# Optimization experiments

Hardware: AMD Instinct MI355X
Metric: run time of the kernel (lower is better)

The kernel has to match this reference:

```python
import jax, jax.numpy as jnp
import numpy as np

B, T, E, NH, VOCAB, MULT = 1, 1024, 768, 12, 32000, 32
N = E * MULT // NH  # 2048
LN_EPS = 1e-5


def setup_inputs() -> dict:
    key = jax.random.key(0)
    ks = jax.random.split(key, 6)
    return {
        "idx": jax.random.randint(ks[0], (B, T), 0, VOCAB),
        "embed": jax.random.normal(ks[1], (VOCAB, E), jnp.float32) * 0.02,
        "encoder": jax.random.normal(ks[2], (NH, E, N), jnp.float32) * 0.02,
        "encoder_v": jax.random.normal(ks[3], (NH, E, N), jnp.float32) * 0.02,
        "decoder": jax.random.normal(ks[4], (NH * N, E), jnp.float32) * 0.02,
        "lm_head": jax.random.normal(ks[5], (VOCAB, E), jnp.float32) * 0.02,
        "ln_w": jnp.ones((E,), jnp.float32),
        "ln_b": jnp.zeros((E,), jnp.float32),
        "n_layer": 6,
    }


def reference(idx, embed, encoder, encoder_v, decoder, lm_head, ln_w, ln_b, n_layer):
    nh, e, n = encoder.shape
    t = idx.shape[1]
    dec = decoder.reshape(nh, n, e)  # flatten order (h, n) -> h*N + n

    def ln(x):
        m = jnp.mean(x, axis=-1, keepdims=True)
        v = jnp.mean(jnp.square(x - m), axis=-1, keepdims=True)
        return (x - m) * jax.lax.rsqrt(v + LN_EPS) * ln_w + ln_b

    causal = jnp.tril(jnp.ones((t, t), bool))  # [T, T]
    scale = 1.0 / np.sqrt(n).astype(np.float32)

    x = ln(embed[idx])  # [B, T, E]  (the unsqueezed head dim broadcasts; keep it squeezed)
    for _ in range(n_layer):
        # encoder projection + ReLU: [B,T,E] x [H,E,N] -> [B,H,T,N]
        x_sparse = jax.nn.relu(jnp.einsum("bte,hen->bhtn", x, encoder))
        # hand-rolled causal attention, Q=K=x_sparse, V=x (broadcast over heads)
        scores = jnp.einsum("bhqn,bhkn->bhqk", x_sparse, x_sparse) * scale
        scores = jnp.where(causal, scores, -jnp.inf)
        attn = jax.nn.softmax(scores, axis=-1)
        y = jnp.einsum("bhqk,bke->bhqe", attn, x)  # [B,H,T,E]
        y = ln(y)
        y_sparse = jax.nn.relu(jnp.einsum("bhte,hen->bhtn", y, encoder_v))
        xy = x_sparse * y_sparse  # [B,H,T,N]; dropout p=0 -> identity
        y_mlp = jnp.einsum("bhtn,hne->bte", xy, dec)  # decoder matmul
        x = ln(x + ln(y_mlp))
    logits = jnp.einsum("bte,ve->btv", x, lm_head)
    return logits
```

## Files before the change

kernel.cpp:

```cpp
#include <hip/hip_runtime.h>

typedef unsigned short u16;
typedef short bf16x8 __attribute__((ext_vector_type(8)));
typedef float f32x4 __attribute__((ext_vector_type(4)));
typedef u16 u16x4 __attribute__((ext_vector_type(4)));

#define TT     1024
#define EE     768
#define NHH    12
#define ND     2048
#define VOC    32000
#define HNN    24576
#define NLAYER 6
#define LN_EPS 1e-5f
#define SPLITK 16

__device__ __forceinline__ float b2f(u16 u){
  unsigned int x = ((unsigned int)u) << 16; float f; __builtin_memcpy(&f, &x, 4); return f;
}
__device__ __forceinline__ u16 f2b(float f){
  unsigned int x; __builtin_memcpy(&x, &f, 4);
  x = x + 0x7fffu + ((x >> 16) & 1u);
  return (u16)(x >> 16);
}

__device__ __forceinline__ void gload16(const void* g, void* lds){
  __builtin_amdgcn_global_load_lds(
      (const __attribute__((address_space(1))) unsigned int*)g,
      (__attribute__((address_space(3))) unsigned int*)(unsigned int)(unsigned long long)lds,
      16, 0, 0);
}

__device__ __forceinline__ bf16x8 ldsr(unsigned addr){
  bf16x8 r;
  asm volatile("ds_read_b128 %0, %1" : "=v"(r) : "v"(addr));
  return r;
}

__device__ __forceinline__ void blk_sum2(float& a, float& b){
  #pragma unroll
  for (int o = 32; o > 0; o >>= 1){ a += __shfl_down(a, o); b += __shfl_down(b, o); }
  __shared__ float sa[4], sb[4];
  int lane = threadIdx.x & 63, wid = threadIdx.x >> 6;
  __syncthreads();
  if (lane == 0){ sa[wid] = a; sb[wid] = b; }
  __syncthreads();
  a = (sa[0] + sa[1]) + (sa[2] + sa[3]);
  b = (sb[0] + sb[1]) + (sb[2] + sb[3]);
}
__device__ __forceinline__ float blk_max(float v){
  #pragma unroll
  for (int o = 32; o > 0; o >>= 1) v = fmaxf(v, __shfl_down(v, o));
  __shared__ float sm[4];
  int lane = threadIdx.x & 63, wid = threadIdx.x >> 6;
  __syncthreads();
  if (lane == 0) sm[wid] = v;
  __syncthreads();
  return fmaxf(fmaxf(sm[0], sm[1]), fmaxf(sm[2], sm[3]));
}
__device__ __forceinline__ float blk_sum(float v){
  #pragma unroll
  for (int o = 32; o > 0; o >>= 1) v += __shfl_down(v, o);
  __shared__ float ss[4];
  int lane = threadIdx.x & 63, wid = threadIdx.x >> 6;
  __syncthreads();
  if (lane == 0) ss[wid] = v;
  __syncthreads();
  return (ss[0] + ss[1]) + (ss[2] + ss[3]);
}

__global__ void prep(const float* __restrict__ enc, const float* __restrict__ encv,
                     const float* __restrict__ dec, const float* __restrict__ lmh,
                     u16* __restrict__ encT, u16* __restrict__ encvT,
                     u16* __restrict__ decT, u16* __restrict__ lmhB){
  __shared__ float tile[32][33];
  int b = blockIdx.x;
  int lx = threadIdx.x & 31, ly = threadIdx.x >> 5;
  if (b < 36864){
    const float* in; u16* out;
    if (b < 18432){ in = enc; out = encT; } else { in = encv; out = encvT; b -= 18432; }
    int z = b / 1536, rem = b - z * 1536;
    int c0 = (rem & 63) * 32, r0 = (rem >> 6) * 32;
    in  += (long)z * EE * ND;
    out += (long)z * ND * EE;
    #pragma unroll
    for (int i = 0; i < 32; i += 8)
      tile[ly + i][lx] = in[(long)(r0 + ly + i) * ND + c0 + lx];
    __syncthreads();
    #pragma unroll
    for (int i = 0; i < 32; i += 8)
      out[(long)(c0 + ly + i) * EE + r0 + lx] = f2b(tile[lx][ly + i]);
  } else if (b < 55296){
    b -= 36864;
    int c0 = (b % 24) * 32, r0 = (b / 24) * 32;
    #pragma unroll
    for (int i = 0; i < 32; i += 8)
      tile[ly + i][lx] = dec[(long)(r0 + ly + i) * EE + c0 + lx];
    __syncthreads();
    #pragma unroll
    for (int i = 0; i < 32; i += 8)
      decT[(long)(c0 + ly + i) * HNN + r0 + lx] = f2b(tile[lx][ly + i]);
  } else {
    b -= 55296;
    long i = ((long)b * 256 + threadIdx.x) * 4;
    float4 v = *(const float4*)(lmh + i);
    u16x4 o; o.x = f2b(v.x); o.y = f2b(v.y); o.z = f2b(v.z); o.w = f2b(v.w);
    *(u16x4*)(lmhB + i) = o;
  }
}

__global__ void xpose(const u16* __restrict__ in, u16* __restrict__ out){
  __shared__ u16 t[64][65];
  int e0 = blockIdx.x * 64, t0 = blockIdx.y * 64;
  int lx = threadIdx.x & 63, ly = threadIdx.x >> 6;
  #pragma unroll
  for (int i = 0; i < 64; i += 4)
    t[ly + i][lx] = in[(long)(t0 + ly + i) * EE + e0 + lx];
  __syncthreads();
  #pragma unroll
  for (int i = 0; i < 64; i += 4)
    out[(long)(e0 + ly + i) * TT + t0 + lx] = t[lx][ly + i];
}

__global__ void embed_ln(const int* __restrict__ idx, const float* __restrict__ emb,
                         const float* __restrict__ w, const float* __restrict__ b,
                         float* __restrict__ xf, u16* __restrict__ xb){
  int t = blockIdx.x, tid = threadIdx.x;
  const float* src = emb + (long)idx[t] * EE;
  float v[4] = {0.f, 0.f, 0.f, 0.f};
  if (tid < 192){
    float4 r = *(const float4*)&src[tid * 4];
    v[0] = r.x; v[1] = r.y; v[2] = r.z; v[3] = r.w;
  }
  float s = (v[0] + v[1]) + (v[2] + v[3]);
  float s2 = (v[0]*v[0] + v[1]*v[1]) + (v[2]*v[2] + v[3]*v[3]);
  blk_sum2(s, s2);
  float m  = s * (1.0f / EE);
  float var = s2 * (1.0f / EE) - m * m;
  float rs = rsqrtf(var + LN_EPS);
  if (tid < 192){
    int e0 = tid * 4;
    float4 o; u16x4 ob;
    float* op = &o.x;
    #pragma unroll
    for (int j = 0; j < 4; j++){
      float ov = (v[j] - m) * rs * w[e0 + j] + b[e0 + j];
      op[j] = ov; ob[j] = f2b(ov);
    }
    *(float4*)&xf[(long)t * EE + e0] = o;
    *(u16x4*)&xb[(long)t * EE + e0] = ob;
  }
}

__global__ void ln_rows(const u16* __restrict__ in, u16* __restrict__ out,
                        const float* __restrict__ w, const float* __restrict__ b){
  long row = blockIdx.x; int tid = threadIdx.x;
  const u16* src = in + row * EE;
  float v[4] = {0.f, 0.f, 0.f, 0.f};
  if (tid < 192){
    u16x4 r = *(const u16x4*)&src[tid * 4];
    #pragma unroll
    for (int j = 0; j < 4; j++) v[j] = b2f(r[j]);
  }
  float s = (v[0] + v[1]) + (v[2] + v[3]);
  float s2 = (v[0]*v[0] + v[1]*v[1]) + (v[2]*v[2] + v[3]*v[3]);
  blk_sum2(s, s2);
  float m = s * (1.0f / EE);
  float var = s2 * (1.0f / EE) - m * m;
  float rs = rsqrtf(var + LN_EPS);
  if (tid < 192){
    int e0 = tid * 4;
    u16x4 ob;
    #pragma unroll
    for (int j = 0; j < 4; j++) ob[j] = f2b((v[j] - m) * rs * w[e0 + j] + b[e0 + j]);
    *(u16x4*)&out[row * EE + e0] = ob;
  }
}

__global__ void softmax_rows(const u16* __restrict__ scores, u16* __restrict__ attn){
  int q = blockIdx.x, h = blockIdx.y, tid = threadIdx.x;
  const u16* srow = scores + ((long)h * TT + q) * TT;
  u16* arow = attn + ((long)h * TT + q) * TT;
  const int len = q + 1;
  const int pad = (q + 128) & ~127;
  u16x4 raw = *(const u16x4*)&srow[tid * 4];
  float v[4];
  float mx = -1e30f;
  #pragma unroll
  for (int j = 0; j < 4; j++){
    int i = tid * 4 + j;
    v[j] = (i < len) ? b2f(raw[j]) : -1e30f;
    mx = fmaxf(mx, v[j]);
  }
  mx = blk_max(mx);
  float s = 0.f;
  #pragma unroll
  for (int j = 0; j < 4; j++){
    int i = tid * 4 + j;
    float e = (i < len) ? __expf(v[j] - mx) : 0.f;
    v[j] = e; s += e;
  }
  float inv = 1.0f / blk_sum(s);
  int i0 = tid * 4;
  if (i0 < pad){
    u16x4 o;
    #pragma unroll
    for (int j = 0; j < 4; j++) o[j] = (i0 + j < len) ? f2b(v[j] * inv) : (u16)0;
    *(u16x4*)&arow[i0] = o;
  }
}

template<int P>
__global__ void residual_ln(const u16* __restrict__ part, const float* __restrict__ xin,
                            float* __restrict__ xf, u16* __restrict__ xb,
                            const float* __restrict__ w, const float* __restrict__ b){
  int t = blockIdx.x, tid = threadIdx.x;
  float g[4] = {0.f, 0.f, 0.f, 0.f};
  if (tid < 192){
    int e0 = tid * 4;
    #pragma unroll
    for (int pp = 0; pp < P; pp++){
      u16x4 r = *(const u16x4*)&part[((long)pp * TT + t) * EE + e0];
      #pragma unroll
      for (int j = 0; j < 4; j++) g[j] += b2f(r[j]);
    }
  }
  float s = (g[0] + g[1]) + (g[2] + g[3]);
  float s2 = (g[0]*g[0] + g[1]*g[1]) + (g[2]*g[2] + g[3]*g[3]);
  blk_sum2(s, s2);
  float m = s * (1.0f / EE), var = s2 * (1.0f / EE) - m * m;
  float rs = rsqrtf(var + LN_EPS);
  float hh[4] = {0.f, 0.f, 0.f, 0.f};
  if (tid < 192){
    int e0 = tid * 4;
    float4 xi = *(const float4*)&xin[(long)t * EE + e0];
    const float* xp = &xi.x;
    #pragma unroll
    for (int j = 0; j < 4; j++)
      hh[j] = xp[j] + ((g[j] - m) * rs * w[e0 + j] + b[e0 + j]);
  }
  s = (hh[0] + hh[1]) + (hh[2] + hh[3]);
  s2 = (hh[0]*hh[0] + hh[1]*hh[1]) + (hh[2]*hh[2] + hh[3]*hh[3]);
  blk_sum2(s, s2);
  m = s * (1.0f / EE); var = s2 * (1.0f / EE) - m * m; rs = rsqrtf(var + LN_EPS);
  if (tid < 192){
    int e0 = tid * 4;
    float4 o; u16x4 ob;
    float* op = &o.x;
    #pragma unroll
    for (int j = 0; j < 4; j++){
      float ov = (hh[j] - m) * rs * w[e0 + j] + b[e0 + j];
      op[j] = ov; ob[j] = f2b(ov);
    }
    *(float4*)&xf[(long)t * EE + e0] = o;
    *(u16x4*)&xb[(long)t * EE + e0] = ob;
  }
}

template<int EPI>
__global__ __launch_bounds__(512, 2)
void g8(const u16* __restrict__ Ab, long sA,
        const u16* __restrict__ Bb, long sB,
        void* __restrict__ Cb, long sC,
        int grid_m, int grid_mn,
        int K, int lda, int ldb, int ldc, float scale,
        const u16* __restrict__ Mul, long sMul, int ldmul){
  __shared__ __align__(16) u16 S[65536];

  const int nwg = gridDim.x, orig = blockIdx.x;
  const int q = nwg >> 3, r = nwg & 7, xcd = orig & 7;
  const int wgid = (xcd < r ? xcd*(q+1) : r*(q+1) + (xcd - r)*q) + (orig >> 3);
  const int z   = wgid / grid_mn;
  const int rem = wgid - z*grid_mn;
  const int nb  = rem / grid_m;
  const int mb  = rem - nb*grid_m;
  const int m0 = mb*256, n0 = nb*256;
  const int tid = threadIdx.x, lane = tid & 63, wid = tid >> 6;

  if (EPI == 2 && n0 > m0 + 255) return;

  const u16* A = Ab + (long)z*sA;
  const u16* B = Bb + (long)z*sB;

  const int rS = wid*16 + (lane >> 2);
  const int cS = (((lane & 3) ^ ((rS >> 1) & 3)) << 3);
  const u16* gA = A + (long)(m0 + rS)*lda + cS;
  const u16* gB = B + (long)(n0 + rS)*ldb + cS;

  char* Sb = (char*)&S[0];
  const unsigned db0 = 0, db1 = 65536u;
  auto issue = [&](const u16* src, unsigned dstOff){
    gload16(src, Sb + dstOff + (unsigned)wid*1024u);
  };

  const int wr = wid >> 2, wc = wid & 3;
  const int fr = lane & 15, fk = lane >> 4;
  const unsigned base = (unsigned)(unsigned long long)Sb;
  unsigned aOff[8], bOff[4];
  #pragma unroll
  for (int mi = 0; mi < 8; mi++){
    int row = wr*128 + mi*16 + fr;
    aOff[mi] = (unsigned)(row*64 + ((fk ^ ((row >> 1) & 3)) << 4));
  }
  #pragma unroll
  for (int ni = 0; ni < 4; ni++){
    int row = wc*64 + ni*16 + fr;
    bOff[ni] = 32768u + (unsigned)(row*64 + ((fk ^ ((row >> 1) & 3)) << 4));
  }

  const int NT = K >> 6;
  const int s0 = ((mb*3 + nb*5 + z)*7) % NT;
  const long lda128 = (long)128*lda, ldb128 = (long)128*ldb;

  f32x4 acc[8][4] = {};

  int p1 = s0 + 1; if (p1 >= NT) p1 -= NT;
  {
    const long kp0 = (long)s0*64, kp1 = (long)p1*64;
    issue(gA + kp0,            db0);          issue(gA + kp0 + lda128,      db0 + 8192u);
    issue(gB + kp0,            db0+32768u);   issue(gB + kp0 + ldb128,      db0 + 40960u);
    issue(gA + kp0 + 32,       db0+16384u);   issue(gA + kp0 + 32 + lda128, db0 + 24576u);
    issue(gB + kp0 + 32,       db0+49152u);   issue(gB + kp0 + 32 + ldb128, db0 + 57344u);
    issue(gA + kp1,            db1);          issue(gA + kp1 + lda128,      db1 + 8192u);
    issue(gB + kp1,            db1+32768u);   issue(gB + kp1 + ldb128,      db1 + 40960u);
  }
  asm volatile("s_waitcnt vmcnt(8)" ::: "memory");
  __builtin_amdgcn_s_barrier();
  __builtin_amdgcn_sched_barrier(0);

  int t1 = p1;
  int t2 = p1 + 1; if (t2 >= NT) t2 -= NT;
  for (int t = 0; t < NT; t++){
    const unsigned cur = (t & 1) ? db1 : db0;
    const unsigned oth = (t & 1) ? db0 : db1;
    const long k1 = (long)t1*64, k2 = (long)t2*64;
    const unsigned d1A = oth + 16384u, d1B = oth + 49152u;
    const unsigned d2A = cur,          d2B = cur + 32768u;
    bf16x8 a[4], b[4];

    #pragma unroll
    for (int ni = 0; ni < 4; ni++) b[ni] = ldsr(base + cur + bOff[ni]);
    #pragma unroll
    for (int u = 0; u < 4; u++)    a[u]  = ldsr(base + cur + aOff[u]);
    issue(gA + k1 + 32, d1A); issue(gA + k1 + 32 + lda128, d1A + 8192u);
    __builtin_amdgcn_s_barrier();
    asm volatile("s_waitcnt lgkmcnt(0)" ::: "memory");
    __builtin_amdgcn_sched_barrier(0);
    __builtin_amdgcn_s_setprio(1);
    #pragma unroll
    for (int u = 0; u < 4; u++)
      #pragma unroll
      for (int ni = 0; ni < 4; ni++)
        acc[u][ni] = __builtin_amdgcn_mfma_f32_16x16x32_bf16(a[u], b[ni], acc[u][ni], 0, 0, 0);
    __builtin_amdgcn_s_setprio(0);
    __builtin_amdgcn_s_barrier();
    __builtin_amdgcn_sched_barrier(0);

    #pragma unroll
    for (int u = 0; u < 4; u++) a[u] = ldsr(base + cur + aOff[4 + u]);
    issue(gB + k1 + 32, d1B); issue(gB + k1 + 32 + ldb128, d1B + 8192u);
    __builtin_amdgcn_s_barrier();
    asm volatile("s_waitcnt lgkmcnt(0)" ::: "memory");
    __builtin_amdgcn_sched_barrier(0);
    __builtin_amdgcn_s_setprio(1);
    #pragma unroll
    for (int u = 0; u < 4; u++)
      #pragma unroll
      for (int ni = 0; ni < 4; ni++)
        acc[4+u][ni] = __builtin_amdgcn_mfma_f32_16x16x32_bf16(a[u], b[ni], acc[4+u][ni], 0, 0, 0);
    __builtin_amdgcn_s_setprio(0);
    asm volatile("s_waitcnt vmcnt(8)" ::: "memory");
    __builtin_amdgcn_s_barrier();
    __builtin_amdgcn_sched_barrier(0);

    #pragma unroll
    for (int ni = 0; ni < 4; ni++) b[ni] = ldsr(base + cur + bOff[ni] + 16384u);
    #pragma unroll
    for (int u = 0; u < 4; u++)    a[u]  = ldsr(base + cur + aOff[u] + 16384u);
    issue(gA + k2, d2A); issue(gA + k2 + lda128, d2A + 8192u);
    __builtin_amdgcn_s_barrier();
    asm volatile("s_waitcnt lgkmcnt(0)" ::: "memory");
    __builtin_amdgcn_sched_barrier(0);
    __builtin_amdgcn_s_setprio(1);
    #pragma unroll
    for (int u = 0; u < 4; u++)
      #pragma unroll
      for (int ni = 0; ni < 4; ni++)
        acc[u][ni] = __builtin_amdgcn_mfma_f32_16x16x32_bf16(a[u], b[ni], acc[u][ni], 0, 0, 0);
    __builtin_amdgcn_s_setprio(0);
    __builtin_amdgcn_s_barrier();
    __builtin_amdgcn_sched_barrier(0);

    #pragma unroll
    for (int u = 0; u < 4; u++) a[u] = ldsr(base + cur + aOff[4 + u] + 16384u);
    issue(gB + k2, d2B); issue(gB + k2 + ldb128, d2B + 8192u);
    __builtin_amdgcn_s_barrier();
    asm volatile("s_waitcnt lgkmcnt(0)" ::: "memory");
    __builtin_amdgcn_sched_barrier(0);
    __builtin_amdgcn_s_setprio(1);
    #pragma unroll
    for (int u = 0; u < 4; u++)
      #pragma unroll
      for (int ni = 0; ni < 4; ni++)
        acc[4+u][ni] = __builtin_amdgcn_mfma_f32_16x16x32_bf16(a[u], b[ni], acc[4+u][ni], 0, 0, 0);
    __builtin_amdgcn_s_setprio(0);
    asm volatile("s_waitcnt vmcnt(8)" ::: "memory");
    __builtin_amdgcn_s_barrier();
    __builtin_amdgcn_sched_barrier(0);

    t1 = t2;
    t2 = t2 + 1; if (t2 >= NT) t2 -= NT;
  }
  asm volatile("s_waitcnt vmcnt(0)" ::: "memory");

  const int er = (lane >> 4) * 4, ec = lane & 15;
  #pragma unroll
  for (int mi = 0; mi < 8; mi++){
    #pragma unroll
    for (int ni = 0; ni < 4; ni++){
      #pragma unroll
      for (int j = 0; j < 4; j++){
        int row = m0 + wr*128 + mi*16 + er + j;
        int col = n0 + wc*64 + ni*16 + ec;
        float v = acc[mi][ni][j];
        if (EPI == 0){
          ((float*)Cb + (long)z * sC)[(long)row * ldc + col] = v;
        } else if (EPI == 1){
          v = v > 0.f ? v : 0.f;
          ((u16*)Cb + (long)z * sC)[(long)row * ldc + col] = f2b(v);
        } else if (EPI == 2){
          ((u16*)Cb + (long)z * sC)[(long)row * ldc + col] = f2b(v * scale);
        } else {
          v = v > 0.f ? v : 0.f;
          float mfv = b2f((Mul + (long)z * sMul)[(long)row * ldmul + col]);
          ((u16*)Cb + (long)z * sC)[(long)row * ldc + col] = f2b(v * mfv);
        }
      }
    }
  }
}

template<int EPI, bool CCLAMP>
__global__ __launch_bounds__(256, 2)
void gemmw(const u16* __restrict__ Ab, long sA,
           const u16* __restrict__ Bb, long sB,
           void* __restrict__ Cb, long sC,
           int grid_m, int grid_mn,
           int K, int lda, int ldb, int ldc){
  constexpr unsigned BUFB = 24576u;
  __shared__ __align__(16) u16 S[3 * 12288];

  const int nwg = gridDim.x, orig = blockIdx.x;
  const int q = nwg >> 3, r = nwg & 7, xcd = orig & 7;
  const int wgid = (xcd < r ? xcd*(q+1) : r*(q+1) + (xcd - r)*q) + (orig >> 3);
  const int z   = wgid / grid_mn;
  const int rem = wgid - z*grid_mn;
  const int nb  = rem / grid_m;
  const int mb  = rem - nb*grid_m;
  const int m0 = mb*128, n0 = nb*256;
  const int tid = threadIdx.x, lane = tid & 63, wid = tid >> 6;

  const u16* A = Ab + (long)z*sA;
  const u16* B = Bb + (long)z*sB;

  const int rS = tid >> 2;
  const int cS = (((tid & 3) ^ ((rS >> 1) & 3)) << 3);
  const u16* gA[2]; const u16* gB[4];
  #pragma unroll
  for (int i = 0; i < 2; i++) gA[i] = A + (long)(m0 + i*64 + rS)*lda + cS;
  #pragma unroll
  for (int i = 0; i < 4; i++) gB[i] = B + (long)(n0 + i*64 + rS)*ldb + cS;

  char* Sb = (char*)&S[0];
  auto stage = [&](int kt, unsigned bB){
    const int ko = kt << 5;
    gload16(gA[0] + ko, Sb + bB +          wid*1024u);
    gload16(gA[1] + ko, Sb + bB +  4096u + wid*1024u);
    #pragma unroll
    for (int i = 0; i < 4; i++)
      gload16(gB[i] + ko, Sb + bB + 8192u + i*4096u + wid*1024u);
  };

  const int wr = wid >> 1, wc = wid & 1;
  const int fr = lane & 15, fk = lane >> 4;
  const unsigned base = (unsigned)(unsigned long long)Sb;
  unsigned aAd[4], bAd[8];
  #pragma unroll
  for (int mi = 0; mi < 4; mi++){
    int row = wr*64 + mi*16 + fr;
    aAd[mi] = base + (unsigned)(row*64 + ((fk ^ ((row >> 1) & 3)) << 4));
  }
  #pragma unroll
  for (int ni = 0; ni < 8; ni++){
    int row = wc*128 + ni*16 + fr;
    bAd[ni] = base + 8192u + (unsigned)(row*64 + ((fk ^ ((row >> 1) & 3)) << 4));
  }

  const int Keff = CCLAMP ? (m0 + 128 < K ? m0 + 128 : K) : K;
  const int NT = Keff >> 5;
  const int s0 = (mb*13 + nb*7 + z*5) % NT;

  f32x4 acc[4][8] = {};

  int p1 = s0 + 1; if (p1 >= NT) p1 -= NT;
  stage(s0, 0);
  stage(p1, BUFB);
  asm volatile("s_waitcnt vmcnt(6)" ::: "memory");
  __builtin_amdgcn_s_barrier();
  __builtin_amdgcn_sched_barrier(0);

  unsigned rbB = 0, wbB = 2u*BUFB;
  for (int t = 0; t < NT; t++){
    int nx = (t + 2 < NT) ? t + 2 : NT - 1;
    int ph = s0 + nx; if (ph >= NT) ph -= NT;
    stage(ph, wbB);
    bf16x8 afr[4], bfr[8];
    #pragma unroll
    for (int ni = 0; ni < 8; ni++) bfr[ni] = ldsr(bAd[ni] + rbB);
    #pragma unroll
    for (int mi = 0; mi < 4; mi++) afr[mi] = ldsr(aAd[mi] + rbB);
    __builtin_amdgcn_s_barrier();
    asm volatile("s_waitcnt lgkmcnt(0)" ::: "memory");
    __builtin_amdgcn_sched_barrier(0);
    __builtin_amdgcn_s_setprio(1);
    #pragma unroll
    for (int mi = 0; mi < 4; mi++)
      #pragma unroll
      for (int ni = 0; ni < 8; ni++)
        acc[mi][ni] = __builtin_amdgcn_mfma_f32_16x16x32_bf16(afr[mi], bfr[ni], acc[mi][ni], 0, 0, 0);
    __builtin_amdgcn_s_setprio(0);
    __builtin_amdgcn_sched_barrier(0);
    asm volatile("s_waitcnt vmcnt(6)" ::: "memory");
    __builtin_amdgcn_s_barrier();
    __builtin_amdgcn_sched_barrier(0);
    unsigned tmp = rbB; rbB += BUFB; if (rbB == 3u*BUFB) rbB = 0;
    wbB = tmp;
  }
  asm volatile("s_waitcnt vmcnt(0)" ::: "memory");

  const int er = (lane >> 4) * 4, ec = lane & 15;
  #pragma unroll
  for (int mi = 0; mi < 4; mi++){
    #pragma unroll
    for (int ni = 0; ni < 8; ni++){
      #pragma unroll
      for (int j = 0; j < 4; j++){
        int row = m0 + wr*64 + mi*16 + er + j;
        int col = n0 + wc*128 + ni*16 + ec;
        float v = acc[mi][ni][j];
        if (EPI == 0){
          ((float*)Cb + (long)z * sC)[(long)row * ldc + col] = v;
        } else {
          ((u16*)Cb + (long)z * sC)[(long)row * ldc + col] = f2b(v);
        }
      }
    }
  }
}

extern "C" void kernel_launch(void* const* d_in, const int* in_sizes, int n_in,
                              void* d_out, int out_size, void* d_ws, size_t ws_size,
                              hipStream_t stream){
  (void)in_sizes; (void)n_in; (void)out_size; (void)ws_size;
  const int*   idx     = (const int*)  d_in[0];
  const float* embed   = (const float*)d_in[1];
  const float* encoder = (const float*)d_in[2];
  const float* encv    = (const float*)d_in[3];
  const float* decoder = (const float*)d_in[4];
  const float* lm_head = (const float*)d_in[5];
  const float* ln_w    = (const float*)d_in[6];
  const float* ln_b    = (const float*)d_in[7];
  float* out = (float*)d_out;

  char* p = (char*)d_ws;
  auto take = [&](size_t n){ char* r = p; p += (n + 255) & ~(size_t)255; return r; };
  u16*   encT  = (u16*)  take((size_t)NHH * ND * EE * 2);
  u16*   encvT = (u16*)  take((size_t)NHH * ND * EE * 2);
  u16*   decT  = (u16*)  take((size_t)EE * HNN * 2);
  u16*   lmhB  = (u16*)  take((size_t)VOC * EE * 2);
  float* xf    = (float*)take((size_t)TT * EE * 4);
  u16*   xb    = (u16*)  take((size_t)TT * EE * 2);
  u16*   xT    = (u16*)  take((size_t)EE * TT * 2);
  u16*   xs    = (u16*)  take((size_t)NHH * TT * ND * 2);
  char*  big   =         take((size_t)NHH * TT * TT * 4);
  u16*   attn  = (u16*)  take((size_t)NHH * TT * TT * 2);
  u16*   yb    = (u16*)  take((size_t)NHH * TT * EE * 2);
  take((size_t)8 * TT * EE * 4);
  u16*   scores = (u16*)big;
  u16*   ybig   = (u16*)big;
  u16*   xy     = (u16*)big;
  u16*   part   = attn;

  dim3 blk(256, 1, 1);

  prep<<<dim3(79296, 1, 1), blk, 0, stream>>>(encoder, encv, decoder, lm_head,
                                              encT, encvT, decT, lmhB);

  embed_ln<<<dim3(TT, 1, 1), blk, 0, stream>>>(idx, embed, ln_w, ln_b, xf, xb);
  xpose<<<dim3(EE / 64, TT / 64, 1), blk, 0, stream>>>(xb, xT);

  const float scl = 0.022097086912079608f;

  for (int L = 0; L < NLAYER; ++L){
    g8<1><<<dim3(4*8*NHH), dim3(512), 0, stream>>>(
        xb, 0, encT, (long)ND * EE, xs, (long)TT * ND,
        4, 32, EE, EE, EE, ND, 0.f, (const u16*)0, 0, 0);
    g8<2><<<dim3(4*4*NHH), dim3(512), 0, stream>>>(
        xs, (long)TT * ND, xs, (long)TT * ND, scores, (long)TT * TT,
        4, 16, ND, ND, ND, TT, scl, (const u16*)0, 0, 0);
    softmax_rows<<<dim3(TT, NHH, 1), blk, 0, stream>>>(scores, attn);
    gemmw<4,true><<<dim3(8*3*NHH), blk, 0, stream>>>(
        attn, (long)TT * TT, xT, 0, ybig, (long)TT * EE,
        8, 24, TT, TT, TT, EE);
    ln_rows<<<dim3(NHH * TT, 1, 1), blk, 0, stream>>>(ybig, yb, ln_w, ln_b);
    g8<3><<<dim3(4*8*NHH), dim3(512), 0, stream>>>(
        yb, (long)TT * EE, encvT, (long)ND * EE, xy, (long)ND,
        4, 32, EE, EE, EE, HNN, 0.f, xs, (long)TT * ND, ND);
    gemmw<4,false><<<dim3(8*3*SPLITK), blk, 0, stream>>>(
        xy, (long)(HNN / SPLITK), decT, (long)(HNN / SPLITK), part, (long)TT * EE,
        8, 24, HNN / SPLITK, HNN, HNN, EE);
    residual_ln<SPLITK><<<dim3(TT, 1, 1), blk, 0, stream>>>(part, xf, xf, xb, ln_w, ln_b);
    xpose<<<dim3(EE / 64, TT / 64, 1), blk, 0, stream>>>(xb, xT);
  }

  g8<0><<<dim3(4*125), dim3(512), 0, stream>>>(
      xb, 0, lmhB, 0, out, 0,
      4, 500, EE, EE, EE, VOC, 0.f, (const u16*)0, 0, 0);
}
```

Baseline: 1.949 ms.

## Vectorize weight-prep transposes with 64x64 tiles and linearize g8 k-loop prefetch

Measured after the change: 1.897 ms. -2.7%, faster.

```diff
diff --git a/kernel.cpp b/kernel.cpp
--- a/kernel.cpp
+++ b/kernel.cpp
@@ -73,35 +73,53 @@
                      const float* __restrict__ dec, const float* __restrict__ lmh,
                      u16* __restrict__ encT, u16* __restrict__ encvT,
                      u16* __restrict__ decT, u16* __restrict__ lmhB){
-  __shared__ float tile[32][33];
+  __shared__ float tile[64][65];
   int b = blockIdx.x;
-  int lx = threadIdx.x & 31, ly = threadIdx.x >> 5;
-  if (b < 36864){
+  int lx = threadIdx.x & 15, ly = threadIdx.x >> 4;
+  if (b < 9216){
     const float* in; u16* out;
-    if (b < 18432){ in = enc; out = encT; } else { in = encv; out = encvT; b -= 18432; }
-    int z = b / 1536, rem = b - z * 1536;
-    int c0 = (rem & 63) * 32, r0 = (rem >> 6) * 32;
+    if (b < 4608){ in = enc; out = encT; } else { in = encv; out = encvT; b -= 4608; }
+    int z = b / 384, rem = b - z * 384;
+    int r0 = (rem >> 5) * 64;
+    int c0 = (rem & 31) * 64;
     in  += (long)z * EE * ND;
     out += (long)z * ND * EE;
     #pragma unroll
-    for (int i = 0; i < 32; i += 8)
-      tile[ly + i][lx] = in[(long)(r0 + ly + i) * ND + c0 + lx];
+    for (int i = 0; i < 4; i++){
+      float4 v = *(const float4*)&in[(long)(r0 + ly + i*16) * ND + c0 + lx*4];
+      tile[lx*4+0][ly+i*16] = v.x; tile[lx*4+1][ly+i*16] = v.y;
+      tile[lx*4+2][ly+i*16] = v.z; tile[lx*4+3][ly+i*16] = v.w;
+    }
     __syncthreads();
     #pragma unroll
-    for (int i = 0; i < 32; i += 8)
-      out[(long)(c0 + ly + i) * EE + r0 + lx] = f2b(tile[lx][ly + i]);
-  } else if (b < 55296){
-    b -= 36864;
-    int c0 = (b % 24) * 32, r0 = (b / 24) * 32;
-    #pragma unroll
-    for (int i = 0; i < 32; i += 8)
-      tile[ly + i][lx] = dec[(long)(r0 + ly + i) * EE + c0 + lx];
+    for (int i = 0; i < 4; i++){
+      int crow = ly + i*16;
+      u16x4 o;
+      #pragma unroll
+      for (int j = 0; j < 4; j++) o[j] = f2b(tile[crow][lx*4+j]);
+      *(u16x4*)&out[(long)(c0 + crow) * EE + r0 + lx*4] = o;
+    }
+  } else if (b < 13824){
+    b -= 9216;
+    int r0 = (b / 12) * 64;
+    int c0 = (b % 12) * 64;
+    #pragma unroll
+    for (int i = 0; i < 4; i++){
+      float4 v = *(const float4*)&dec[(long)(r0 + ly + i*16) * EE + c0 + lx*4];
+      tile[lx*4+0][ly+i*16] = v.x; tile[lx*4+1][ly+i*16] = v.y;
+      tile[lx*4+2][ly+i*16] = v.z; tile[lx*4+3][ly+i*16] = v.w;
+    }
     __syncthreads();
     #pragma unroll
-    for (int i = 0; i < 32; i += 8)
-      decT[(long)(c0 + ly + i) * HNN + r0 + lx] = f2b(tile[lx][ly + i]);
+    for (int i = 0; i < 4; i++){
+      int crow = ly + i*16;
+      u16x4 o;
+      #pragma unroll
+      for (int j = 0; j < 4; j++) o[j] = f2b(tile[crow][lx*4+j]);
+      *(u16x4*)&decT[(long)(c0 + crow) * HNN + r0 + lx*4] = o;
+    }
   } else {
-    b -= 55296;
+    b -= 13824;
     long i = ((long)b * 256 + threadIdx.x) * 4;
     float4 v = *(const float4*)(lmh + i);
     u16x4 o; o.x = f2b(v.x); o.y = f2b(v.y); o.z = f2b(v.z); o.w = f2b(v.w);
@@ -265,7 +283,7 @@
         int grid_m, int grid_mn,
         int K, int lda, int ldb, int ldc, float scale,
         const u16* __restrict__ Mul, long sMul, int ldmul){
-  __shared__ __align__(16) u16 S[65536];
+  __shared__ __align__(16) u16 S[69632];
 
   const int nwg = gridDim.x, orig = blockIdx.x;
   const int q = nwg >> 3, r = nwg & 7, xcd = orig & 7;
@@ -288,7 +306,7 @@
   const u16* gB = B + (long)(n0 + rS)*ldb + cS;
 
   char* Sb = (char*)&S[0];
-  const unsigned db0 = 0, db1 = 65536u;
+  const unsigned db0 = 0, db1 = 65536u, scr = 131072u;
   auto issue = [&](const u16* src, unsigned dstOff){
     gload16(src, Sb + dstOff + (unsigned)wid*1024u);
   };
@@ -309,33 +327,30 @@
   }
 
   const int NT = K >> 6;
-  const int s0 = ((mb*3 + nb*5 + z)*7) % NT;
   const long lda128 = (long)128*lda, ldb128 = (long)128*ldb;
 
   f32x4 acc[8][4] = {};
 
-  int p1 = s0 + 1; if (p1 >= NT) p1 -= NT;
-  {
-    const long kp0 = (long)s0*64, kp1 = (long)p1*64;
-    issue(gA + kp0,            db0);          issue(gA + kp0 + lda128,      db0 + 8192u);
-    issue(gB + kp0,            db0+32768u);   issue(gB + kp0 + ldb128,      db0 + 40960u);
-    issue(gA + kp0 + 32,       db0+16384u);   issue(gA + kp0 + 32 + lda128, db0 + 24576u);
-    issue(gB + kp0 + 32,       db0+49152u);   issue(gB + kp0 + 32 + ldb128, db0 + 57344u);
-    issue(gA + kp1,            db1);          issue(gA + kp1 + lda128,      db1 + 8192u);
-    issue(gB + kp1,            db1+32768u);   issue(gB + kp1 + ldb128,      db1 + 40960u);
-  }
+  issue(gA,              db0);          issue(gA + lda128,          db0 + 8192u);
+  issue(gB,              db0+32768u);   issue(gB + ldb128,          db0 + 40960u);
+  issue(gA + 32,         db0+16384u);   issue(gA + 32 + lda128,     db0 + 24576u);
+  issue(gB + 32,         db0+49152u);   issue(gB + 32 + ldb128,     db0 + 57344u);
+  issue(gA + 64,         db1);          issue(gA + 64 + lda128,     db1 + 8192u);
+  issue(gB + 64,         db1+32768u);   issue(gB + 64 + ldb128,     db1 + 40960u);
   asm volatile("s_waitcnt vmcnt(8)" ::: "memory");
   __builtin_amdgcn_s_barrier();
   __builtin_amdgcn_sched_barrier(0);
 
-  int t1 = p1;
-  int t2 = p1 + 1; if (t2 >= NT) t2 -= NT;
   for (int t = 0; t < NT; t++){
     const unsigned cur = (t & 1) ? db1 : db0;
     const unsigned oth = (t & 1) ? db0 : db1;
-    const long k1 = (long)t1*64, k2 = (long)t2*64;
-    const unsigned d1A = oth + 16384u, d1B = oth + 49152u;
-    const unsigned d2A = cur,          d2B = cur + 32768u;
+    const bool v1 = (t + 1 < NT), v2 = (t + 2 < NT);
+    const long k1 = (long)(v1 ? t + 1 : 0) * 64;
+    const long k2 = (long)(v2 ? t + 2 : 0) * 64;
+    const unsigned d1A = v1 ? oth + 16384u : scr;
+    const unsigned d1B = v1 ? oth + 49152u : scr;
+    const unsigned d2A = v2 ? cur           : scr;
+    const unsigned d2B = v2 ? cur + 32768u  : scr;
     bf16x8 a[4], b[4];
 
     #pragma unroll
@@ -407,9 +422,6 @@
     asm volatile("s_waitcnt vmcnt(8)" ::: "memory");
     __builtin_amdgcn_s_barrier();
     __builtin_amdgcn_sched_barrier(0);
-
-    t1 = t2;
-    t2 = t2 + 1; if (t2 >= NT) t2 -= NT;
   }
   asm volatile("s_waitcnt vmcnt(0)" ::: "memory");
 
@@ -593,7 +605,7 @@
 
   dim3 blk(256, 1, 1);
 
-  prep<<<dim3(79296, 1, 1), blk, 0, stream>>>(encoder, encv, decoder, lm_head,
+  prep<<<dim3(37824, 1, 1), blk, 0, stream>>>(encoder, encv, decoder, lm_head,
                                               encT, encvT, decT, lmhB);
 
   embed_ln<<<dim3(TT, 1, 1), blk, 0, stream>>>(idx, embed, ln_w, ln_b, xf, xb);
```
